# Kernel optimization log

Hardware: AMD Instinct MI355X
Metric: run time of the kernel (lower is better)

Reference implementation:

```python
import jax, jax.numpy as jnp
import numpy as np

NEG = -9.0e15
D = 768


def _init_params(key, d):
    ks = jax.random.split(key, 12)
    s = 0.02
    p = {}
    p['Wa'] = jax.random.normal(ks[0], (d, 1), jnp.float32) * s
    p['ba'] = jnp.zeros((1,), jnp.float32)
    for i, name in enumerate(['qs', 'ks', 'qc', 'kc', 'qr', 'kr']):
        p['W' + name] = jax.random.normal(ks[1 + i], (d, d), jnp.float32) * s
        p['b' + name] = jnp.zeros((d,), jnp.float32)
    p['Wf1'] = jax.random.normal(ks[8], (3 * d, d), jnp.float32) * s
    p['bf1'] = jnp.zeros((d,), jnp.float32)
    p['Wf2'] = jax.random.normal(ks[9], (d, d), jnp.float32) * s
    p['bf2'] = jnp.zeros((d,), jnp.float32)
    p['gamma'] = jnp.ones((d,), jnp.float32)
    p['beta'] = jnp.zeros((d,), jnp.float32)
    return p


def setup_inputs() -> dict:
    key = jax.random.key(0)
    k1, k2, k3 = jax.random.split(key, 3)
    B, L = 8, 1024
    inp = {
        'x': jax.random.normal(k1, (B, L, D), jnp.float32),
        'x_ids': jax.random.randint(k2, (B, L), 0, 1000, jnp.int64 if jax.config.read('jax_enable_x64') else jnp.int32).astype(jnp.int32),
        'pad_idx': 0,
    }
    inp.update(_init_params(k3, D))
    return inp


def _forward(x, x_ids, pad_idx, Wa, ba, Wqs, bqs, Wks, bks, Wqc, bqc, Wkc, bkc,
             Wqr, bqr, Wkr, bkr, Wf1, bf1, Wf2, bf2, gamma, beta):
    B, L, d = x.shape
    valid = x_ids != pad_idx                             # [B,L]
    valid_len = valid.sum(axis=1)
    sep_pos = jnp.clip(valid_len // 2, 1, max(1, L - 2))  # [B]
    pos = jnp.arange(L)[None, :]                          # [1,L]
    false_mask = (pos < sep_pos[:, None]) & valid         # [B,L]
    option_mask = (pos > sep_pos[:, None]) & valid        # [B,L]

    # anomaly gate over false segment
    a_logits = (x @ Wa + ba)[..., 0]                      # [B,L]
    a_logits = jnp.where(false_mask, a_logits, NEG)
    gate = jax.nn.softmax(a_logits, axis=1) * false_mask.astype(x.dtype)
    gate = gate / jnp.clip(gate.sum(axis=1, keepdims=True), 1e-8)

    scale = 1.0 / jnp.sqrt(jnp.asarray(d, x.dtype))
    q_sup, k_sup = x @ Wqs + bqs, x @ Wks + bks
    q_con, k_con = x @ Wqc + bqc, x @ Wkc + bkc
    q_rep, k_rep = x @ Wqr + bqr, x @ Wkr + bkr

    sup_s = jnp.einsum('bld,bmd->blm', q_sup, k_sup) * scale
    con_s = jnp.einsum('bld,bmd->blm', q_con, k_con) * scale
    rep_s = jnp.einsum('bld,bmd->blm', q_rep, k_rep) * scale

    pair_mask = false_mask[:, :, None] & option_mask[:, None, :]  # [B,L,L]
    sup_attn = jax.nn.softmax(jnp.where(pair_mask, sup_s, NEG), axis=-1)
    rep_attn = jax.nn.softmax(jnp.where(pair_mask, rep_s + jnp.tanh(con_s), NEG), axis=-1)

    rep_vec = jnp.einsum('blm,bmd->bld', rep_attn, x)
    sup_vec = jnp.einsum('blm,bmd->bld', sup_attn, x)

    anomaly_false = jnp.einsum('bl,bld->bd', gate, x)
    w_rep = jnp.einsum('bl,bld->bd', gate, rep_vec)
    w_sup = jnp.einsum('bl,bld->bd', gate, sup_vec)

    fused = jnp.concatenate([anomaly_false, w_rep, w_sup], axis=-1)
    fused = jnp.maximum(fused @ Wf1 + bf1, 0.0) @ Wf2 + bf2  # dropout = eval identity

    mu = fused.mean(axis=-1, keepdims=True)
    var = ((fused - mu) ** 2).mean(axis=-1, keepdims=True)
    fused = (fused - mu) / jnp.sqrt(var + 1e-5) * gamma + beta
    return fused


def reference(x, x_ids, pad_idx, Wa, ba, Wqs, bqs, Wks, bks, Wqc, bqc, Wkc, bkc,
              Wqr, bqr, Wkr, bkr, Wf1, bf1, Wf2, bf2, gamma, beta):
    return _forward(x, x_ids, pad_idx, Wa, ba, Wqs, bqs, Wks, bks, Wqc, bqc,
                    Wkc, bkc, Wqr, bqr, Wkr, bkr, Wf1, bf1, Wf2, bf2, gamma, beta)
```

## Files before the change

### kernel.cpp

```cpp
#include <hip/hip_runtime.h>
#include <math.h>

#define L 1024
#define NB 8
#define D 768
#define NEGV (-9.0e15f)
#define SCALE 0.036084391824351615f

typedef unsigned short u16;
typedef __attribute__((ext_vector_type(8))) short short8;
typedef __attribute__((ext_vector_type(4))) float float4v;
#define MFMA_BF16 __builtin_amdgcn_mfma_f32_16x16x32_bf16

__device__ __forceinline__ float b2f(u16 u) {
    union { unsigned int i; float f; } v; v.i = ((unsigned int)u) << 16; return v.f;
}
__device__ __forceinline__ u16 f2b(float f) {
    union { float fv; unsigned int i; } v; v.fv = f;
    unsigned int x = v.i;
    x += 0x7fffu + ((x >> 16) & 1u);
    return (u16)(x >> 16);
}

template<int F32>
__device__ __forceinline__ float4 ld4(const void* p, size_t idx) {
    if (F32) return *(const float4*)((const float*)p + idx);
    ushort4 v = *(const ushort4*)((const u16*)p + idx);
    return make_float4(b2f(v.x), b2f(v.y), b2f(v.z), b2f(v.w));
}
template<int F32>
__device__ __forceinline__ float ld1(const void* p, size_t idx) {
    if (F32) return ((const float*)p)[idx];
    return b2f(((const u16*)p)[idx]);
}
__device__ __forceinline__ int ldid(const int* p, size_t idx, int is64) {
    return is64 ? p[idx * 2] : p[idx];
}

#define WS_FLAG  ((size_t)0)
#define WS_SEP   ((size_t)64)
#define WS_C0    ((size_t)128)
#define WS_Z0    ((size_t)192)
#define WS_W1    ((size_t)9472)
#define WS_GATE  ((size_t)18752)
#define WS_CSUP  ((size_t)51520)
#define WS_CREP  ((size_t)84288)
#define WS_AF    ((size_t)117056)
#define WS_WREP  ((size_t)141632)
#define WS_WSUP  ((size_t)166208)
#define WS_HACC  ((size_t)190784)
#define WS_ALOG  ((size_t)215360)
#define WS_T     ((size_t)248128)
#define WS_OACC  ((size_t)303104)
#define WS_XB    ((size_t)524288)
#define WS_Z     ((size_t)13107200)
#define WS_SSUP  ((size_t)31981568)
#define WS_WB    WS_SSUP
#define WS_SCMB  ((size_t)40370176)
#define WS_M     WS_SCMB

struct PP { const void* W[6]; const void* b[6]; };

__global__ __launch_bounds__(128) void kdetect(const void* x, const void* ids, int* flag) {
    __shared__ int cnt[2];
    int tid = threadIdx.x;
    if (tid == 0) { cnt[0] = 0; cnt[1] = 0; }
    __syncthreads();
    if (tid < 64) {
        u16 u = ((const u16*)x)[tid * 2];
        int e = (u >> 7) & 0xFF;
        if (e >= 100 && e <= 140) atomicAdd(&cnt[0], 1);
    } else {
        int v = ((const int*)ids)[(tid - 64) * 2 + 1];
        if (v != 0) atomicAdd(&cnt[1], 1);
    }
    __syncthreads();
    if (tid == 0) {
        flag[0] = (cnt[0] < 32) ? 1 : 0;
        flag[1] = (cnt[1] == 0) ? 1 : 0;
    }
}

template<int F32> __device__ void kbias_body(const void* W, const void* vec,
        float* out, float* vs) {
    int tid = threadIdx.x;
    for (int i = tid; i < D; i += 256) vs[i] = ld1<F32>(vec, i);
    __syncthreads();
    int row = blockIdx.x * 64 + (tid >> 2);
    int sub = tid & 3;
    float acc = 0.f;
    for (int i = 0; i < 48; ++i) {
        int k = i * 16 + sub * 4;
        float4 wv = ld4<F32>(W, (size_t)row * D + k);
        acc += wv.x * vs[k] + wv.y * vs[k + 1] + wv.z * vs[k + 2] + wv.w * vs[k + 3];
    }
    acc += __shfl_xor(acc, 1);
    acc += __shfl_xor(acc, 2);
    if (sub == 0) out[row] = acc;
}
template<int F32> __device__ void kc0_body(const void* bq, const void* bk,
        float* c0, float* red) {
    int tid = threadIdx.x;
    float s = 0.f;
    for (int i = tid; i < D; i += 256) s += ld1<F32>(bq, i) * ld1<F32>(bk, i);
    red[tid] = s; __syncthreads();
    for (int st = 128; st > 0; st >>= 1) { if (tid < st) red[tid] += red[tid + st]; __syncthreads(); }
    if (tid == 0) c0[0] = red[0];
}
__global__ __launch_bounds__(256) void kbias_row(PP pp, float* z0, float* w1,
        float* c0, const int* flag) {
    __shared__ float vs[D];
    __shared__ float red[256];
    int y = blockIdx.y;
    if (y == 4) {
        if (blockIdx.x != 0) return;
        if (flag[0]) kc0_body<1>(pp.b[2], pp.b[3], c0, red);
        else         kc0_body<0>(pp.b[2], pp.b[3], c0, red);
        return;
    }
    const void* W; const void* vec; float* out;
    if (y < 3) { W = pp.W[2 * y + 1]; vec = pp.b[2 * y]; out = z0 + y * D; }
    else       { W = pp.W[2];         vec = pp.b[3];     out = w1; }
    if (flag[0]) kbias_body<1>(W, vec, out, vs);
    else         kbias_body<0>(W, vec, out, vs);
}

template<int F32> __device__ void kx_body(const void* x, const void* Wa,
        const void* ba, const float* w1, const float* c0, u16* xb, float* alog,
        float* tbuf, float* ws2) {
    int tid = threadIdx.x;
    for (int i = tid; i < D; i += 256) {
        ws2[i]     = ld1<F32>(Wa, i);
        ws2[D + i] = w1[i];
    }
    __syncthreads();
    int row = blockIdx.x * 32 + (tid >> 3);
    int sub = tid & 7;
    float a0 = 0.f, a1 = 0.f;
    for (int i = 0; i < 24; ++i) {
        int k = i * 32 + sub * 4;
        float4 xv = ld4<F32>(x, (size_t)row * D + k);
        ushort4 o;
        o.x = f2b(xv.x); o.y = f2b(xv.y); o.z = f2b(xv.z); o.w = f2b(xv.w);
        *(ushort4*)(xb + (size_t)row * D + k) = o;
        a0 += xv.x * ws2[k] + xv.y * ws2[k + 1] + xv.z * ws2[k + 2] + xv.w * ws2[k + 3];
        a1 += xv.x * ws2[D + k] + xv.y * ws2[D + k + 1] + xv.z * ws2[D + k + 2] + xv.w * ws2[D + k + 3];
    }
    #pragma unroll
    for (int d = 1; d < 8; d <<= 1) {
        a0 += __shfl_xor(a0, d); a1 += __shfl_xor(a1, d);
    }
    int b = row >> 10, l = row & 1023;
    if (sub == 0) alog[row] = a0 + ld1<F32>(ba, 0);
    else if (sub == 1 && l < 512) tbuf[(size_t)b * 512 + l] = a1 + c0[0];
}
__global__ __launch_bounds__(256) void kx(const void* x, PP pp, const void* Wa,
        const void* ba, const float* w1, const float* c0, u16* xb, u16* Wb,
        float* alog, float* tbuf, const int* flag) {
    __shared__ float ws2[2 * D];
    int bid = blockIdx.x;
    if (bid < 256) {
        if (flag[0]) kx_body<1>(x, Wa, ba, w1, c0, xb, alog, tbuf, ws2);
        else         kx_body<0>(x, Wa, ba, w1, c0, xb, alog, tbuf, ws2);
        return;
    }
    int t = (bid - 256) / 288, inner = (bid - 256) % 288;
    const void* src = pp.W[t];
    u16* dst = Wb + (size_t)t * D * D;
    size_t base = ((size_t)inner * 256 + threadIdx.x) * 8;
    if (flag[0]) {
        float4 a = *(const float4*)((const float*)src + base);
        float4 b = *(const float4*)((const float*)src + base + 4);
        uint4 o; u16* po = (u16*)&o;
        po[0] = f2b(a.x); po[1] = f2b(a.y); po[2] = f2b(a.z); po[3] = f2b(a.w);
        po[4] = f2b(b.x); po[5] = f2b(b.y); po[6] = f2b(b.z); po[7] = f2b(b.w);
        *(uint4*)(dst + base) = o;
    } else {
        *(uint4*)(dst + base) = *(const uint4*)((const u16*)src + base);
    }
}

__global__ __launch_bounds__(256) void k0b(const int* __restrict__ ids,
        const int* __restrict__ padp, const float* __restrict__ alog,
        float* __restrict__ gate, int* __restrict__ sepArr,
        float* __restrict__ af, float* __restrict__ wrep, float* __restrict__ wsup,
        float* __restrict__ hacc, float* __restrict__ oacc,
        float* __restrict__ csup, float* __restrict__ crep,
        const int* __restrict__ flag) {
    __shared__ float red[256];
    __shared__ int sepSh;
    int is64 = flag[1];
    int b = blockIdx.x, tid = threadIdx.x;
    int pad = padp[0];
    int cnt = 0;
    for (int l = tid; l < L; l += 256) cnt += (ldid(ids, (size_t)b * L + l, is64) != pad) ? 1 : 0;
    red[tid] = (float)cnt; __syncthreads();
    for (int s = 128; s > 0; s >>= 1) { if (tid < s) red[tid] += red[tid + s]; __syncthreads(); }
    if (tid == 0) {
        int vl = (int)red[0];
        int sep = vl / 2; if (sep < 1) sep = 1; if (sep > L - 2) sep = L - 2;
        sepSh = sep; sepArr[b] = sep;
    }
    __syncthreads();
    int sep = sepSh;
    float lv[4]; int lidx[4];
    float mx = -3.4e38f;
    for (int u = 0; u < 4; ++u) {
        int l = tid + u * 256; lidx[u] = l;
        bool fm = (l < sep) && (ldid(ids, (size_t)b * L + l, is64) != pad);
        float v = fm ? alog[b * L + l] : NEGV;
        lv[u] = v; mx = fmaxf(mx, v);
    }
    red[tid] = mx; __syncthreads();
    for (int s = 128; s > 0; s >>= 1) { if (tid < s) red[tid] = fmaxf(red[tid], red[tid + s]); __syncthreads(); }
    mx = red[0]; __syncthreads();
    float se = 0.f;
    for (int u = 0; u < 4; ++u) { lv[u] = expf(lv[u] - mx); se += lv[u]; }
    red[tid] = se; __syncthreads();
    for (int s = 128; s > 0; s >>= 1) { if (tid < s) red[tid] += red[tid + s]; __syncthreads(); }
    float den = fmaxf(red[0], 1e-30f); __syncthreads();
    float gs = 0.f; float gv[4];
    for (int u = 0; u < 4; ++u) {
        int l = lidx[u];
        bool fm = (l < sep) && (ldid(ids, (size_t)b * L + l, is64) != pad);
        float p = lv[u] / den;
        gv[u] = fm ? p : 0.f;
        gs += gv[u];
    }
    red[tid] = gs; __syncthreads();
    for (int s = 128; s > 0; s >>= 1) { if (tid < s) red[tid] += red[tid + s]; __syncthreads(); }
    gs = red[0];
    float inv = 1.f / fmaxf(gs, 1e-8f);
    for (int u = 0; u < 4; ++u) gate[b * L + lidx[u]] = gv[u] * inv;
    for (int l = tid; l < L; l += 256) { csup[b * L + l] = 0.f; crep[b * L + l] = 0.f; }
    for (int i = tid; i < D; i += 256) {
        af[b * D + i] = 0.f; wrep[b * D + i] = 0.f; wsup[b * D + i] = 0.f;
        hacc[b * D + i] = 0.f; oacc[b * D + i] = 0.f;
    }
}

__device__ __forceinline__ void stage128_async(const u16* __restrict__ G, size_t ld,
        int r0, int k0, u16* S, int tid) {
    int rowa = tid >> 2, koa = (tid & 3) << 3;
    int wave = tid >> 6;
    const u16* g1 = &G[(size_t)(r0 + rowa) * ld + k0 + koa];
    const u16* g2 = &G[(size_t)(r0 + rowa + 64) * ld + k0 + koa];
    __builtin_amdgcn_global_load_lds((__attribute__((address_space(1))) void*)(u16*)g1,
        (__attribute__((address_space(3))) void*)(S + wave * 512), 16, 0, 0);
    __builtin_amdgcn_global_load_lds((__attribute__((address_space(1))) void*)(u16*)g2,
        (__attribute__((address_space(3))) void*)(S + 2048 + wave * 512), 16, 0, 0);
}
__device__ __forceinline__ void stage64_async(const u16* __restrict__ G, size_t ld,
        int r0, int k0, u16* S, int tid) {
    int rowa = tid >> 2, koa = (tid & 3) << 3;
    int wave = tid >> 6;
    const u16* g = &G[(size_t)(r0 + rowa) * ld + k0 + koa];
    __builtin_amdgcn_global_load_lds((__attribute__((address_space(1))) void*)(u16*)g,
        (__attribute__((address_space(3))) void*)(S + wave * 512), 16, 0, 0);
}

__device__ __forceinline__ void gemm_core128(const u16* __restrict__ A, size_t lda, int r0,
        const u16* __restrict__ B, size_t ldb, int c0, int K,
        u16* As, u16* Bs, float4v acc[4][4]) {
    int tid = threadIdx.x;
    int lane = tid & 63, wave = tid >> 6;
    int wm = (wave >> 1) << 6, wn = (wave & 1) << 6;
    int quad = lane >> 4, lrow = lane & 15;
    #pragma unroll
    for (int i = 0; i < 4; ++i)
        #pragma unroll
        for (int j = 0; j < 4; ++j) acc[i][j] = (float4v){0.f, 0.f, 0.f, 0.f};
    for (int k0 = 0; k0 < K; k0 += 64) {
        __syncthreads();
        stage128_async(A, lda, r0, k0, As, tid);
        stage128_async(A, lda, r0, k0 + 32, As + 4096, tid);
        stage128_async(B, ldb, c0, k0, Bs, tid);
        stage128_async(B, ldb, c0, k0 + 32, Bs + 4096, tid);
        __syncthreads();
        #pragma unroll
        for (int p = 0; p < 2; ++p) {
            const u16* Ap = As + p * 4096;
            const u16* Bp = Bs + p * 4096;
            short8 af[4], bf[4];
            #pragma unroll
            for (int i = 0; i < 4; ++i) af[i] = *(const short8*)&Ap[(wm + i * 16 + lrow) * 32 + quad * 8];
            #pragma unroll
            for (int j = 0; j < 4; ++j) bf[j] = *(const short8*)&Bp[(wn + j * 16 + lrow) * 32 + quad * 8];
            #pragma unroll
            for (int i = 0; i < 4; ++i)
                #pragma unroll
                for (int j = 0; j < 4; ++j)
                    acc[i][j] = MFMA_BF16(af[i], bf[j], acc[i][j], 0, 0, 0);
        }
    }
}

__device__ __forceinline__ void gemm_core64(const u16* __restrict__ A, size_t lda, int r0,
        const u16* __restrict__ B, size_t ldb, int c0, int K,
        u16* As, u16* Bs, float4v acc[2][4]) {
    int tid = threadIdx.x;
    int lane = tid & 63, wave = tid >> 6;
    int wm = (wave >> 1) << 5, wn = (wave & 1) << 6;
    int quad = lane >> 4, lrow = lane & 15;
    #pragma unroll
    for (int i = 0; i < 2; ++i)
        #pragma unroll
        for (int j = 0; j < 4; ++j) acc[i][j] = (float4v){0.f, 0.f, 0.f, 0.f};
    for (int k0 = 0; k0 < K; k0 += 64) {
        __syncthreads();
        stage64_async(A, lda, r0, k0, As, tid);
        stage64_async(A, lda, r0, k0 + 32, As + 2048, tid);
        stage128_async(B, ldb, c0, k0, Bs, tid);
        stage128_async(B, ldb, c0, k0 + 32, Bs + 4096, tid);
        __syncthreads();
        #pragma unroll
        for (int p = 0; p < 2; ++p) {
            const u16* Ap = As + p * 2048;
            const u16* Bp = Bs + p * 4096;
            short8 fa[2], fb[4];
            #pragma unroll
            for (int i = 0; i < 2; ++i) fa[i] = *(const short8*)&Ap[(wm + i * 16 + lrow) * 32 + quad * 8];
            #pragma unroll
            for (int j = 0; j < 4; ++j) fb[j] = *(const short8*)&Bp[(wn + j * 16 + lrow) * 32 + quad * 8];
            #pragma unroll
            for (int i = 0; i < 2; ++i)
                #pragma unroll
                for (int j = 0; j < 4; ++j)
                    acc[i][j] = MFMA_BF16(fa[i], fb[j], acc[i][j], 0, 0, 0);
        }
    }
}

__global__ __launch_bounds__(256) void kM_mfma(const u16* __restrict__ Wb, u16* __restrict__ Mt) {
    __shared__ __align__(16) u16 As[128 * 64];
    __shared__ __align__(16) u16 Bs[128 * 64];
    int p = blockIdx.z;
    int r0 = blockIdx.y * 128, c0 = blockIdx.x * 128;
    float4v acc[4][4];
    gemm_core128(Wb + (size_t)(2 * p + 1) * D * D, D, r0,
                 Wb + (size_t)(2 * p) * D * D, D, c0, D, As, Bs, acc);
    int lane = threadIdx.x & 63, wave = threadIdx.x >> 6;
    int wm = (wave >> 1) << 6, wn = (wave & 1) << 6;
    int quad = lane >> 4, lrow = lane & 15;
    u16* out = Mt + (size_t)p * D * D;
    #pragma unroll
    for (int i = 0; i < 4; ++i)
        #pragma unroll
        for (int j = 0; j < 4; ++j) {
            int brow = r0 + wm + i * 16 + quad * 4;
            int col = c0 + wn + j * 16 + lrow;
            #pragma unroll
            for (int r = 0; r < 4; ++r)
                out[(size_t)(brow + r) * D + col] = f2b(acc[i][j][r]);
        }
}

__global__ __launch_bounds__(256) void kZ_mfma(const u16* __restrict__ xb,
        const u16* __restrict__ Mt, const float* __restrict__ z0,
        u16* __restrict__ Zbuf, const int* __restrict__ sepArr) {
    __shared__ __align__(16) u16 As[64 * 64];
    __shared__ __align__(16) u16 Bs[128 * 64];
    int z = blockIdx.z;
    int p = z >> 3, b = z & 7;
    int sep = sepArr[b];
    int r0 = blockIdx.y * 64;
    if (r0 >= sep) return;
    int c0 = blockIdx.x * 128;
    float4v acc[2][4];
    gemm_core64(xb + (size_t)b * L * D, D, r0,
                Mt + (size_t)p * D * D, D, c0, D, As, Bs, acc);
    int lane = threadIdx.x & 63, wave = threadIdx.x >> 6;
    int wm = (wave >> 1) << 5, wn = (wave & 1) << 6;
    int quad = lane >> 4, lrow = lane & 15;
    const float* z0p = z0 + p * D;
    u16* out = Zbuf + ((size_t)p * NB + b) * 512 * D;
    #pragma unroll
    for (int i = 0; i < 2; ++i)
        #pragma unroll
        for (int j = 0; j < 4; ++j) {
            int brow = r0 + wm + i * 16 + quad * 4;
            int col = c0 + wn + j * 16 + lrow;
            float zb = z0p[col];
            #pragma unroll
            for (int r = 0; r < 4; ++r)
                out[(size_t)(brow + r) * D + col] = f2b(acc[i][j][r] + zb);
        }
}

__global__ __launch_bounds__(256) void kS_mfma(const u16* __restrict__ Zbuf,
        const u16* __restrict__ xb, const float* __restrict__ tcbuf,
        const int* __restrict__ sepArr, u16* __restrict__ ssup,
        u16* __restrict__ scmb) {
    __shared__ __align__(16) u16 smem[16384];
    int b = blockIdx.z;
    int sep = sepArr[b];
    int xi = blockIdx.x;
    int tid = threadIdx.x, lane = tid & 63, wave = tid >> 6;
    int quad = lane >> 4, lrow = lane & 15;
    int wm = (wave >> 1) << 5, wn = (wave & 1) << 6;
    int m0 = blockIdx.y * 128;
    if (m0 + 127 <= sep) return;
    u16* A0 = smem;
    u16* A1 = smem + 4096;
    u16* Bs = smem + 8192;
    const u16* X = xb + (size_t)b * L * D;
    if (xi < 8) {
        int l0 = xi * 64;
        if (l0 >= sep) return;
        float4v acc[2][4];
        gemm_core64(Zbuf + (size_t)b * 512 * D, D, l0, X, D, m0, D, A0, Bs, acc);
        u16* out = ssup + (size_t)b * 512 * L;
        #pragma unroll
        for (int i = 0; i < 2; ++i)
            #pragma unroll
            for (int j = 0; j < 4; ++j) {
                int brow = l0 + wm + i * 16 + quad * 4;
                int col = m0 + wn + j * 16 + lrow;
                #pragma unroll
                for (int r = 0; r < 4; ++r)
                    out[(size_t)(brow + r) * L + col] = f2b(acc[i][j][r] * SCALE);
            }
        return;
    }
    int l0 = (xi - 8) * 64;
    if (l0 >= sep) return;
    const u16* Zr = Zbuf + ((size_t)2 * NB + b) * 512 * D;
    const u16* Zc = Zbuf + ((size_t)1 * NB + b) * 512 * D;
    float4v ar_[2][4], ac_[2][4];
    #pragma unroll
    for (int i = 0; i < 2; ++i)
        #pragma unroll
        for (int j = 0; j < 4; ++j) { ar_[i][j] = (float4v){0.f,0.f,0.f,0.f}; ac_[i][j] = (float4v){0.f,0.f,0.f,0.f}; }
    for (int k0 = 0; k0 < D; k0 += 64) {
        __syncthreads();
        stage64_async(Zr, D, l0, k0, A0, tid);
        stage64_async(Zr, D, l0, k0 + 32, A0 + 2048, tid);
        stage64_async(Zc, D, l0, k0, A1, tid);
        stage64_async(Zc, D, l0, k0 + 32, A1 + 2048, tid);
        stage128_async(X, D, m0, k0, Bs, tid);
        stage128_async(X, D, m0, k0 + 32, Bs + 4096, tid);
        __syncthreads();
        #pragma unroll
        for (int p = 0; p < 2; ++p) {
            const u16* Arp = A0 + p * 2048;
            const u16* Acp = A1 + p * 2048;
            const u16* Bp  = Bs + p * 4096;
            short8 fr[2], fc[2], fb[4];
            #pragma unroll
            for (int i = 0; i < 2; ++i) {
                fr[i] = *(const short8*)&Arp[(wm + i * 16 + lrow) * 32 + quad * 8];
                fc[i] = *(const short8*)&Acp[(wm + i * 16 + lrow) * 32 + quad * 8];
            }
            #pragma unroll
            for (int j = 0; j < 4; ++j) fb[j] = *(const short8*)&Bp[(wn + j * 16 + lrow) * 32 + quad * 8];
            #pragma unroll
            for (int i = 0; i < 2; ++i)
                #pragma unroll
                for (int j = 0; j < 4; ++j) {
                    ar_[i][j] = MFMA_BF16(fr[i], fb[j], ar_[i][j], 0, 0, 0);
                    ac_[i][j] = MFMA_BF16(fc[i], fb[j], ac_[i][j], 0, 0, 0);
                }
        }
    }
    const float* tc = tcbuf + (size_t)b * 512;
    u16* out = scmb + (size_t)b * 512 * L;
    #pragma unroll
    for (int i = 0; i < 2; ++i)
        #pragma unroll
        for (int j = 0; j < 4; ++j) {
            int brow = l0 + wm + i * 16 + quad * 4;
            int col = m0 + wn + j * 16 + lrow;
            #pragma unroll
            for (int r = 0; r < 4; ++r) {
                float vv = ar_[i][j][r] * SCALE
                         + tanhf((ac_[i][j][r] + tc[brow + r]) * SCALE);
                out[(size_t)(brow + r) * L + col] = f2b(vv);
            }
        }
}

__global__ __launch_bounds__(256) void k2bc(const u16* __restrict__ ssup,
        const u16* __restrict__ scmb, const int* __restrict__ ids,
        const int* __restrict__ padp, const int* __restrict__ sepArr,
        const float* __restrict__ gate, float* __restrict__ csup,
        float* __restrict__ crep, const int* __restrict__ flag) {
    __shared__ float colacc[4][2][1024];
    int b = blockIdx.y;
    int sep = sepArr[b];
    int l0 = blockIdx.x * 8;
    int tid = threadIdx.x, lane = tid & 63, w = tid >> 6;
    for (int i = tid; i < 4 * 2 * 1024; i += 256) ((float*)colacc)[i] = 0.f;
    __syncthreads();
    if (l0 < sep) {
        int is64 = flag[1];
        int pad = padp[0];
        unsigned int okmask = 0;
        #pragma unroll
        for (int u = 0; u < 16; ++u) {
            int m = u * 64 + lane;
            bool ok = (m > sep) && (ldid(ids, (size_t)b * L + m, is64) != pad);
            okmask |= (ok ? 1u : 0u) << u;
        }
        for (int t = 0; t < 2; ++t) {
            int l = l0 + w * 2 + t;
            if (l >= sep) continue;
            float g = gate[b * L + l];
            if (g == 0.f) continue;
            const u16* rs = ssup + ((size_t)b * 512 + l) * L;
            const u16* rc = scmb + ((size_t)b * 512 + l) * L;
            float s0[16], s1[16];
            float mx0 = -3.4e38f, mx1 = -3.4e38f;
            #pragma unroll
            for (int u = 0; u < 16; ++u) {
                int m = u * 64 + lane;
                bool ok = (okmask >> u) & 1u;
                s0[u] = ok ? b2f(rs[m]) : NEGV;
                s1[u] = ok ? b2f(rc[m]) : NEGV;
                mx0 = fmaxf(mx0, s0[u]); mx1 = fmaxf(mx1, s1[u]);
            }
            #pragma unroll
            for (int d = 1; d < 64; d <<= 1) {
                mx0 = fmaxf(mx0, __shfl_xor(mx0, d));
                mx1 = fmaxf(mx1, __shfl_xor(mx1, d));
            }
            float e0 = 0.f, e1 = 0.f;
            #pragma unroll
            for (int u = 0; u < 16; ++u) {
                s0[u] = expf(s0[u] - mx0); e0 += s0[u];
                s1[u] = expf(s1[u] - mx1); e1 += s1[u];
            }
            #pragma unroll
            for (int d = 1; d < 64; d <<= 1) {
                e0 += __shfl_xor(e0, d);
                e1 += __shfl_xor(e1, d);
            }
            float i0 = g / fmaxf(e0, 1e-30f), i1 = g / fmaxf(e1, 1e-30f);
            #pragma unroll
            for (int u = 0; u < 16; ++u) {
                int m = u * 64 + lane;
                colacc[w][0][m] += s0[u] * i0;
                colacc[w][1][m] += s1[u] * i1;
            }
        }
    }
    __syncthreads();
    for (int m = tid; m < 1024; m += 256) {
        float a0 = colacc[0][0][m] + colacc[1][0][m] + colacc[2][0][m] + colacc[3][0][m];
        float a1 = colacc[0][1][m] + colacc[1][1][m] + colacc[2][1][m] + colacc[3][1][m];
        if (a0 != 0.f) atomicAdd(&csup[b * L + m], a0);
        if (a1 != 0.f) atomicAdd(&crep[b * L + m], a1);
    }
}

__global__ __launch_bounds__(256) void k3(const u16* __restrict__ xb,
        const float* __restrict__ gate, const float* __restrict__ csup,
        const float* __restrict__ crep, float* __restrict__ af,
        float* __restrict__ wrep, float* __restrict__ wsup) {
    int b = blockIdx.y, c = blockIdx.x;
    int tid = threadIdx.x;
    float a0 = 0.f, a1 = 0.f, a2 = 0.f;
    float r0 = 0.f, r1 = 0.f, r2 = 0.f;
    float q0 = 0.f, q1 = 0.f, q2 = 0.f;
    for (int mm = 0; mm < 16; ++mm) {
        int m = c * 16 + mm;
        float wg = gate[b * L + m], wr = crep[b * L + m], wq = csup[b * L + m];
        if (wg == 0.f && wr == 0.f && wq == 0.f) continue;
        size_t base = ((size_t)b * L + m) * D;
        float x0 = b2f(xb[base + tid]);
        float x1 = b2f(xb[base + tid + 256]);
        float x2 = b2f(xb[base + tid + 512]);
        a0 += wg * x0; a1 += wg * x1; a2 += wg * x2;
        r0 += wr * x0; r1 += wr * x1; r2 += wr * x2;
        q0 += wq * x0; q1 += wq * x1; q2 += wq * x2;
    }
    atomicAdd(&af[b * D + tid], a0); atomicAdd(&af[b * D + tid + 256], a1); atomicAdd(&af[b * D + tid + 512], a2);
    atomicAdd(&wrep[b * D + tid], r0); atomicAdd(&wrep[b * D + tid + 256], r1); atomicAdd(&wrep[b * D + tid + 512], r2);
    atomicAdd(&wsup[b * D + tid], q0); atomicAdd(&wsup[b * D + tid + 256], q1); atomicAdd(&wsup[b * D + tid + 512], q2);
}

template<int F32> __device__ void kh1_body(const float* af, const float* wrep,
        const float* wsup, const void* Wf1, float* hacc, float* fs) {
    int tid = threadIdx.x;
    int c0 = blockIdx.x * 128, k0 = blockIdx.y * 144;
    for (int e = tid; e < 8 * 144; e += 256) {
        int b = e / 144, kk = e - b * 144;
        int k = k0 + kk;
        float v = (k < D) ? af[b * D + k] : (k < 2 * D) ? wrep[b * D + k - D]
                                                        : wsup[b * D + k - 2 * D];
        fs[b * 144 + kk] = v;
    }
    __syncthreads();
    int col = c0 + (tid & 127);
    int kg = tid >> 7;
    float acc[NB];
    #pragma unroll
    for (int b = 0; b < NB; ++b) acc[b] = 0.f;
    #pragma unroll 4
    for (int r = 0; r < 72; ++r) {
        int kk = kg * 72 + r;
        float w = ld1<F32>(Wf1, (size_t)(k0 + kk) * D + col);
        #pragma unroll
        for (int b = 0; b < NB; ++b) acc[b] += fs[b * 144 + kk] * w;
    }
    #pragma unroll
    for (int b = 0; b < NB; ++b) atomicAdd(&hacc[b * D + col], acc[b]);
}
__global__ __launch_bounds__(256) void kh1(const float* af, const float* wrep,
        const float* wsup, const void* Wf1, float* hacc, const int* flag) {
    __shared__ float fs[8 * 144];
    if (flag[0]) kh1_body<1>(af, wrep, wsup, Wf1, hacc, fs);
    else         kh1_body<0>(af, wrep, wsup, Wf1, hacc, fs);
}

template<int F32> __device__ void kh2_body(const float* hacc, const void* bf1,
        const void* Wf2, float* oacc, float* hsl) {
    int tid = threadIdx.x;
    int c0 = blockIdx.x * 128, k0 = blockIdx.y * 96;
    for (int e = tid; e < 8 * 96; e += 256) {
        int b = e / 96, kk = e - b * 96;
        int k = k0 + kk;
        hsl[b * 96 + kk] = fmaxf(hacc[b * D + k] + ld1<F32>(bf1, k), 0.f);
    }
    __syncthreads();
    int col = c0 + (tid & 127);
    int kg = tid >> 7;
    float acc[NB];
    #pragma unroll
    for (int b = 0; b < NB; ++b) acc[b] = 0.f;
    #pragma unroll 4
    for (int r = 0; r < 48; ++r) {
        int kk = kg * 48 + r;
        float w = ld1<F32>(Wf2, (size_t)(k0 + kk) * D + col);
        #pragma unroll
        for (int b = 0; b < NB; ++b) acc[b] += hsl[b * 96 + kk] * w;
    }
    #pragma unroll
    for (int b = 0; b < NB; ++b) atomicAdd(&oacc[b * D + col], acc[b]);
}
__global__ __launch_bounds__(256) void kh2(const float* hacc, const void* bf1,
        const void* Wf2, float* oacc, const int* flag) {
    __shared__ float hsl[8 * 96];
    if (flag[0]) kh2_body<1>(hacc, bf1, Wf2, oacc, hsl);
    else         kh2_body<0>(hacc, bf1, Wf2, oacc, hsl);
}

template<int F32> __device__ void kln_body(const float* oacc, const void* bf2,
        const void* gamma, const void* beta, void* out, float* red) {
    int b = blockIdx.x, tid = threadIdx.x;
    float o[3];
    #pragma unroll
    for (int u = 0; u < 3; ++u) {
        int i = tid + u * 256;
        o[u] = oacc[b * D + i] + ld1<F32>(bf2, i);
    }
    red[tid] = o[0] + o[1] + o[2]; __syncthreads();
    for (int s = 128; s > 0; s >>= 1) { if (tid < s) red[tid] += red[tid + s]; __syncthreads(); }
    float mu = red[0] / (float)D; __syncthreads();
    float vs = 0.f;
    #pragma unroll
    for (int u = 0; u < 3; ++u) vs += (o[u] - mu) * (o[u] - mu);
    red[tid] = vs; __syncthreads();
    for (int s = 128; s > 0; s >>= 1) { if (tid < s) red[tid] += red[tid + s]; __syncthreads(); }
    float var = red[0] / (float)D;
    float rstd = 1.0f / sqrtf(var + 1e-5f);
    #pragma unroll
    for (int u = 0; u < 3; ++u) {
        int i = tid + u * 256;
        float v = (o[u] - mu) * rstd * ld1<F32>(gamma, i) + ld1<F32>(beta, i);
        if (F32) ((float*)out)[b * D + i] = v;
        else     ((u16*)out)[b * D + i] = f2b(v);
    }
}
__global__ __launch_bounds__(256) void kln(const float* oacc, const void* bf2,
        const void* gamma, const void* beta, void* out, const int* flag) {
    __shared__ float red[256];
    if (flag[0]) kln_body<1>(oacc, bf2, gamma, beta, out, red);
    else         kln_body<0>(oacc, bf2, gamma, beta, out, red);
}

extern "C" void kernel_launch(void* const* d_in, const int* in_sizes, int n_in,
                              void* d_out, int out_size, void* d_ws, size_t ws_size,
                              hipStream_t stream) {
    const void* x    = d_in[0];
    const int* ids   = (const int*)d_in[1];
    const int* padp  = (const int*)d_in[2];
    const void* Wa   = d_in[3];
    const void* ba   = d_in[4];
    PP pp;
    pp.W[0] = d_in[5];  pp.b[0] = d_in[6];
    pp.W[1] = d_in[7];  pp.b[1] = d_in[8];
    pp.W[2] = d_in[9];  pp.b[2] = d_in[10];
    pp.W[3] = d_in[11]; pp.b[3] = d_in[12];
    pp.W[4] = d_in[13]; pp.b[4] = d_in[14];
    pp.W[5] = d_in[15]; pp.b[5] = d_in[16];
    const void* Wf1 = d_in[17]; const void* bf1 = d_in[18];
    const void* Wf2 = d_in[19]; const void* bf2 = d_in[20];
    const void* gamma = d_in[21]; const void* beta = d_in[22];

    char* ws = (char*)d_ws;
    int*   flag   = (int*)(ws + WS_FLAG);
    int*   sepArr = (int*)(ws + WS_SEP);
    float* c0   = (float*)(ws + WS_C0);
    float* z0   = (float*)(ws + WS_Z0);
    float* w1   = (float*)(ws + WS_W1);
    float* gate = (float*)(ws + WS_GATE);
    float* csup = (float*)(ws + WS_CSUP);
    float* crep = (float*)(ws + WS_CREP);
    float* af   = (float*)(ws + WS_AF);
    float* wrep = (float*)(ws + WS_WREP);
    float* wsup = (float*)(ws + WS_WSUP);
    float* hacc = (float*)(ws + WS_HACC);
    float* oacc = (float*)(ws + WS_OACC);
    float* alog = (float*)(ws + WS_ALOG);
    float* tbuf = (float*)(ws + WS_T);
    u16* xb   = (u16*)(ws + WS_XB);
    u16* Zbuf = (u16*)(ws + WS_Z);
    u16* Wb   = (u16*)(ws + WS_WB);
    u16* Mt   = (u16*)(ws + WS_M);
    u16* ssup = (u16*)(ws + WS_SSUP);
    u16* scmb = (u16*)(ws + WS_SCMB);

    kdetect<<<dim3(1), dim3(128), 0, stream>>>(x, ids, flag);
    kbias_row<<<dim3(12, 5), dim3(256), 0, stream>>>(pp, z0, w1, c0, flag);
    kx<<<dim3(1984), dim3(256), 0, stream>>>(x, pp, Wa, ba, w1, c0, xb, Wb, alog, tbuf, flag);
    k0b<<<dim3(NB), dim3(256), 0, stream>>>(ids, padp, alog, gate, sepArr,
                                            af, wrep, wsup, hacc, oacc, csup, crep, flag);
    kM_mfma<<<dim3(6, 6, 3), dim3(256), 0, stream>>>(Wb, Mt);
    kZ_mfma<<<dim3(6, 8, 24), dim3(256), 0, stream>>>(xb, Mt, z0, Zbuf, sepArr);
    kS_mfma<<<dim3(16, 8, NB), dim3(256), 0, stream>>>(Zbuf, xb, tbuf, sepArr, ssup, scmb);
    k2bc<<<dim3(64, NB), dim3(256), 0, stream>>>(ssup, scmb, ids, padp, sepArr,
                                                 gate, csup, crep, flag);
    k3<<<dim3(64, NB), dim3(256), 0, stream>>>(xb, gate, csup, crep, af, wrep, wsup);
    kh1<<<dim3(6, 16), dim3(256), 0, stream>>>(af, wrep, wsup, Wf1, hacc, flag);
    kh2<<<dim3(6, 8), dim3(256), 0, stream>>>(hacc, bf1, Wf2, oacc, flag);
    kln<<<dim3(NB), dim3(256), 0, stream>>>(oacc, bf2, gamma, beta, d_out, flag);
}
```

Before: 279.6 us.

## Fuse launch chain, inline dtype detection, double-buffer MFMA GEMMs

Removes the separate detect kernel: every kernel now recomputes the dtype flags with a wave ballot. kbias_row is merged into kx as extra blocks, and kM is merged into k0b as kB. The GEMMs now double-buffer their async global-to-LDS staging to overlap loads with MFMA. kS computes the sup and combined score tiles in one pass, sharing the x operand, with fewer grid blocks. This cuts launch count and serial dependencies, but every kernel pays a redundant detection read and the fused kernels have heterogeneous blocks.

```diff
diff --git a/kernel.cpp b/kernel.cpp
--- a/kernel.cpp
+++ b/kernel.cpp
@@ -35,6 +35,22 @@
 }
 __device__ __forceinline__ int ldid(const int* p, size_t idx, int is64) {
     return is64 ? p[idx * 2] : p[idx];
+}
+
+__device__ __forceinline__ void detect2(const void* x, const void* ids, int* sh) {
+    int tid = threadIdx.x;
+    if (tid < 64) {
+        u16 u = ((const u16*)x)[tid * 2];
+        int e = (u >> 7) & 0xFF;
+        unsigned long long balf = __ballot(e >= 100 && e <= 140);
+        int v = ((const int*)ids)[tid * 2 + 1];
+        unsigned long long bali = __ballot(v != 0);
+        if (tid == 0) {
+            sh[0] = (__popcll(balf) < 32) ? 1 : 0;
+            sh[1] = (bali == 0ULL) ? 1 : 0;
+        }
+    }
+    __syncthreads();
 }
 
 #define WS_FLAG  ((size_t)0)
@@ -61,32 +77,12 @@
 
 struct PP { const void* W[6]; const void* b[6]; };
 
-__global__ __launch_bounds__(128) void kdetect(const void* x, const void* ids, int* flag) {
-    __shared__ int cnt[2];
-    int tid = threadIdx.x;
-    if (tid == 0) { cnt[0] = 0; cnt[1] = 0; }
-    __syncthreads();
-    if (tid < 64) {
-        u16 u = ((const u16*)x)[tid * 2];
-        int e = (u >> 7) & 0xFF;
-        if (e >= 100 && e <= 140) atomicAdd(&cnt[0], 1);
-    } else {
-        int v = ((const int*)ids)[(tid - 64) * 2 + 1];
-        if (v != 0) atomicAdd(&cnt[1], 1);
-    }
-    __syncthreads();
-    if (tid == 0) {
-        flag[0] = (cnt[0] < 32) ? 1 : 0;
-        flag[1] = (cnt[1] == 0) ? 1 : 0;
-    }
-}
-
 template<int F32> __device__ void kbias_body(const void* W, const void* vec,
-        float* out, float* vs) {
+        float* out, float* vs, float* red, int xi) {
     int tid = threadIdx.x;
     for (int i = tid; i < D; i += 256) vs[i] = ld1<F32>(vec, i);
     __syncthreads();
-    int row = blockIdx.x * 64 + (tid >> 2);
+    int row = xi * 64 + (tid >> 2);
     int sub = tid & 3;
     float acc = 0.f;
     for (int i = 0; i < 48; ++i) {
@@ -107,36 +103,15 @@
     for (int st = 128; st > 0; st >>= 1) { if (tid < st) red[tid] += red[tid + st]; __syncthreads(); }
     if (tid == 0) c0[0] = red[0];
 }
-__global__ __launch_bounds__(256) void kbias_row(PP pp, float* z0, float* w1,
-        float* c0, const int* flag) {
-    __shared__ float vs[D];
-    __shared__ float red[256];
-    int y = blockIdx.y;
-    if (y == 4) {
-        if (blockIdx.x != 0) return;
-        if (flag[0]) kc0_body<1>(pp.b[2], pp.b[3], c0, red);
-        else         kc0_body<0>(pp.b[2], pp.b[3], c0, red);
-        return;
-    }
-    const void* W; const void* vec; float* out;
-    if (y < 3) { W = pp.W[2 * y + 1]; vec = pp.b[2 * y]; out = z0 + y * D; }
-    else       { W = pp.W[2];         vec = pp.b[3];     out = w1; }
-    if (flag[0]) kbias_body<1>(W, vec, out, vs);
-    else         kbias_body<0>(W, vec, out, vs);
-}
 
 template<int F32> __device__ void kx_body(const void* x, const void* Wa,
-        const void* ba, const float* w1, const float* c0, u16* xb, float* alog,
-        float* tbuf, float* ws2) {
-    int tid = threadIdx.x;
-    for (int i = tid; i < D; i += 256) {
-        ws2[i]     = ld1<F32>(Wa, i);
-        ws2[D + i] = w1[i];
-    }
+        const void* ba, u16* xb, float* alog, float* ws2) {
+    int tid = threadIdx.x;
+    for (int i = tid; i < D; i += 256) ws2[i] = ld1<F32>(Wa, i);
     __syncthreads();
     int row = blockIdx.x * 32 + (tid >> 3);
     int sub = tid & 7;
-    float a0 = 0.f, a1 = 0.f;
+    float a0 = 0.f;
     for (int i = 0; i < 24; ++i) {
         int k = i * 32 + sub * 4;
         float4 xv = ld4<F32>(x, (size_t)row * D + k);
@@ -144,53 +119,219 @@
         o.x = f2b(xv.x); o.y = f2b(xv.y); o.z = f2b(xv.z); o.w = f2b(xv.w);
         *(ushort4*)(xb + (size_t)row * D + k) = o;
         a0 += xv.x * ws2[k] + xv.y * ws2[k + 1] + xv.z * ws2[k + 2] + xv.w * ws2[k + 3];
-        a1 += xv.x * ws2[D + k] + xv.y * ws2[D + k + 1] + xv.z * ws2[D + k + 2] + xv.w * ws2[D + k + 3];
-    }
-    #pragma unroll
-    for (int d = 1; d < 8; d <<= 1) {
-        a0 += __shfl_xor(a0, d); a1 += __shfl_xor(a1, d);
-    }
-    int b = row >> 10, l = row & 1023;
+    }
+    #pragma unroll
+    for (int d = 1; d < 8; d <<= 1) a0 += __shfl_xor(a0, d);
     if (sub == 0) alog[row] = a0 + ld1<F32>(ba, 0);
-    else if (sub == 1 && l < 512) tbuf[(size_t)b * 512 + l] = a1 + c0[0];
-}
-__global__ __launch_bounds__(256) void kx(const void* x, PP pp, const void* Wa,
-        const void* ba, const float* w1, const float* c0, u16* xb, u16* Wb,
-        float* alog, float* tbuf, const int* flag) {
-    __shared__ float ws2[2 * D];
+}
+__global__ __launch_bounds__(256) void kx(const void* x, const int* ids, PP pp,
+        const void* Wa, const void* ba, u16* xb, u16* Wb, float* alog,
+        float* z0, float* w1, float* c0f) {
+    __shared__ float sf[2 * D];
+    __shared__ int fsh[2];
+    detect2(x, ids, fsh);
+    int F32 = fsh[0];
     int bid = blockIdx.x;
     if (bid < 256) {
-        if (flag[0]) kx_body<1>(x, Wa, ba, w1, c0, xb, alog, tbuf, ws2);
-        else         kx_body<0>(x, Wa, ba, w1, c0, xb, alog, tbuf, ws2);
+        if (F32) kx_body<1>(x, Wa, ba, xb, alog, sf);
+        else     kx_body<0>(x, Wa, ba, xb, alog, sf);
         return;
     }
-    int t = (bid - 256) / 288, inner = (bid - 256) % 288;
-    const void* src = pp.W[t];
-    u16* dst = Wb + (size_t)t * D * D;
-    size_t base = ((size_t)inner * 256 + threadIdx.x) * 8;
-    if (flag[0]) {
-        float4 a = *(const float4*)((const float*)src + base);
-        float4 b = *(const float4*)((const float*)src + base + 4);
-        uint4 o; u16* po = (u16*)&o;
-        po[0] = f2b(a.x); po[1] = f2b(a.y); po[2] = f2b(a.z); po[3] = f2b(a.w);
-        po[4] = f2b(b.x); po[5] = f2b(b.y); po[6] = f2b(b.z); po[7] = f2b(b.w);
-        *(uint4*)(dst + base) = o;
-    } else {
-        *(uint4*)(dst + base) = *(const uint4*)((const u16*)src + base);
-    }
-}
-
-__global__ __launch_bounds__(256) void k0b(const int* __restrict__ ids,
+    if (bid < 1984) {
+        int t = (bid - 256) / 288, inner = (bid - 256) % 288;
+        const void* src = pp.W[t];
+        u16* dst = Wb + (size_t)t * D * D;
+        size_t base = ((size_t)inner * 256 + threadIdx.x) * 8;
+        if (F32) {
+            float4 a = *(const float4*)((const float*)src + base);
+            float4 b = *(const float4*)((const float*)src + base + 4);
+            uint4 o; u16* po = (u16*)&o;
+            po[0] = f2b(a.x); po[1] = f2b(a.y); po[2] = f2b(a.z); po[3] = f2b(a.w);
+            po[4] = f2b(b.x); po[5] = f2b(b.y); po[6] = f2b(b.z); po[7] = f2b(b.w);
+            *(uint4*)(dst + base) = o;
+        } else {
+            *(uint4*)(dst + base) = *(const uint4*)((const u16*)src + base);
+        }
+        return;
+    }
+    int i = bid - 1984;
+    int y = i / 12, xi = i % 12;
+    float* vs = sf;
+    float* red = sf + D;
+    if (y == 4) {
+        if (xi != 0) return;
+        if (F32) kc0_body<1>(pp.b[2], pp.b[3], c0f, red);
+        else     kc0_body<0>(pp.b[2], pp.b[3], c0f, red);
+        return;
+    }
+    const void* W; const void* vec; float* out;
+    if (y < 3) { W = pp.W[2 * y + 1]; vec = pp.b[2 * y]; out = z0 + y * D; }
+    else       { W = pp.W[2];         vec = pp.b[3];     out = w1; }
+    if (F32) kbias_body<1>(W, vec, out, vs, red, xi);
+    else     kbias_body<0>(W, vec, out, vs, red, xi);
+}
+
+__device__ __forceinline__ void stage128_async(const u16* __restrict__ G, size_t ld,
+        int r0, int k0, u16* S, int tid) {
+    int rowa = tid >> 2, koa = (tid & 3) << 3;
+    int wave = tid >> 6;
+    const u16* g1 = &G[(size_t)(r0 + rowa) * ld + k0 + koa];
+    const u16* g2 = &G[(size_t)(r0 + rowa + 64) * ld + k0 + koa];
+    __builtin_amdgcn_global_load_lds((__attribute__((address_space(1))) void*)(u16*)g1,
+        (__attribute__((address_space(3))) void*)(S + wave * 512), 16, 0, 0);
+    __builtin_amdgcn_global_load_lds((__attribute__((address_space(1))) void*)(u16*)g2,
+        (__attribute__((address_space(3))) void*)(S + 2048 + wave * 512), 16, 0, 0);
+}
+__device__ __forceinline__ void stage64_async(const u16* __restrict__ G, size_t ld,
+        int r0, int k0, u16* S, int tid) {
+    int rowa = tid >> 2, koa = (tid & 3) << 3;
+    int wave = tid >> 6;
+    const u16* g = &G[(size_t)(r0 + rowa) * ld + k0 + koa];
+    __builtin_amdgcn_global_load_lds((__attribute__((address_space(1))) void*)(u16*)g,
+        (__attribute__((address_space(3))) void*)(S + wave * 512), 16, 0, 0);
+}
+
+__device__ __forceinline__ void gemm64_db(const u16* __restrict__ A, size_t lda, int r0,
+        const u16* __restrict__ B, size_t ldb, int c0, int K,
+        u16* As, u16* Bs, float4v acc[2][4]) {
+    int tid = threadIdx.x;
+    int lane = tid & 63, wave = tid >> 6;
+    int wm = (wave >> 1) << 5, wn = (wave & 1) << 6;
+    int quad = lane >> 4, lrow = lane & 15;
+    #pragma unroll
+    for (int i = 0; i < 2; ++i)
+        #pragma unroll
+        for (int j = 0; j < 4; ++j) acc[i][j] = (float4v){0.f, 0.f, 0.f, 0.f};
+    stage64_async(A, lda, r0, 0, As, tid);
+    stage64_async(A, lda, r0, 32, As + 2048, tid);
+    stage128_async(B, ldb, c0, 0, Bs, tid);
+    stage128_async(B, ldb, c0, 32, Bs + 4096, tid);
+    __syncthreads();
+    int nt = K >> 6;
+    for (int t = 0; t < nt; ++t) {
+        int cur = t & 1;
+        if (t + 1 < nt) {
+            int k0 = (t + 1) << 6;
+            u16* Ad = As + (cur ^ 1) * 4096;
+            u16* Bd = Bs + (cur ^ 1) * 8192;
+            stage64_async(A, lda, r0, k0, Ad, tid);
+            stage64_async(A, lda, r0, k0 + 32, Ad + 2048, tid);
+            stage128_async(B, ldb, c0, k0, Bd, tid);
+            stage128_async(B, ldb, c0, k0 + 32, Bd + 4096, tid);
+        }
+        const u16* Ab = As + cur * 4096;
+        const u16* Bb = Bs + cur * 8192;
+        #pragma unroll
+        for (int p = 0; p < 2; ++p) {
+            const u16* Ap = Ab + p * 2048;
+            const u16* Bp = Bb + p * 4096;
+            short8 fa[2], fb[4];
+            #pragma unroll
+            for (int i = 0; i < 2; ++i) fa[i] = *(const short8*)&Ap[(wm + i * 16 + lrow) * 32 + quad * 8];
+            #pragma unroll
+            for (int j = 0; j < 4; ++j) fb[j] = *(const short8*)&Bp[(wn + j * 16 + lrow) * 32 + quad * 8];
+            #pragma unroll
+            for (int i = 0; i < 2; ++i)
+                #pragma unroll
+                for (int j = 0; j < 4; ++j)
+                    acc[i][j] = MFMA_BF16(fa[i], fb[j], acc[i][j], 0, 0, 0);
+        }
+        __syncthreads();
+    }
+}
+
+__device__ __forceinline__ void gemm128_db(const u16* __restrict__ A, size_t lda, int r0,
+        const u16* __restrict__ B, size_t ldb, int c0, int K,
+        u16* As, u16* Bs, float4v acc[4][4]) {
+    int tid = threadIdx.x;
+    int lane = tid & 63, wave = tid >> 6;
+    int wm = (wave >> 1) << 6, wn = (wave & 1) << 6;
+    int quad = lane >> 4, lrow = lane & 15;
+    #pragma unroll
+    for (int i = 0; i < 4; ++i)
+        #pragma unroll
+        for (int j = 0; j < 4; ++j) acc[i][j] = (float4v){0.f, 0.f, 0.f, 0.f};
+    stage128_async(A, lda, r0, 0, As, tid);
+    stage128_async(A, lda, r0, 32, As + 4096, tid);
+    stage128_async(B, ldb, c0, 0, Bs, tid);
+    stage128_async(B, ldb, c0, 32, Bs + 4096, tid);
+    __syncthreads();
+    int nt = K >> 6;
+    for (int t = 0; t < nt; ++t) {
+        int cur = t & 1;
+        if (t + 1 < nt) {
+            int k0 = (t + 1) << 6;
+            u16* Ad = As + (cur ^ 1) * 8192;
+            u16* Bd = Bs + (cur ^ 1) * 8192;
+            stage128_async(A, lda, r0, k0, Ad, tid);
+            stage128_async(A, lda, r0, k0 + 32, Ad + 4096, tid);
+            stage128_async(B, ldb, c0, k0, Bd, tid);
+            stage128_async(B, ldb, c0, k0 + 32, Bd + 4096, tid);
+        }
+        const u16* Ab = As + cur * 8192;
+        const u16* Bb = Bs + cur * 8192;
+        #pragma unroll
+        for (int p = 0; p < 2; ++p) {
+            const u16* Ap = Ab + p * 4096;
+            const u16* Bp = Bb + p * 4096;
+            short8 fa[4], fb[4];
+            #pragma unroll
+            for (int i = 0; i < 4; ++i) fa[i] = *(const short8*)&Ap[(wm + i * 16 + lrow) * 32 + quad * 8];
+            #pragma unroll
+            for (int j = 0; j < 4; ++j) fb[j] = *(const short8*)&Bp[(wn + j * 16 + lrow) * 32 + quad * 8];
+            #pragma unroll
+            for (int i = 0; i < 4; ++i)
+                #pragma unroll
+                for (int j = 0; j < 4; ++j)
+                    acc[i][j] = MFMA_BF16(fa[i], fb[j], acc[i][j], 0, 0, 0);
+        }
+        __syncthreads();
+    }
+}
+
+__global__ __launch_bounds__(256) void kB(const void* x, const int* __restrict__ ids,
         const int* __restrict__ padp, const float* __restrict__ alog,
         float* __restrict__ gate, int* __restrict__ sepArr,
         float* __restrict__ af, float* __restrict__ wrep, float* __restrict__ wsup,
         float* __restrict__ hacc, float* __restrict__ oacc,
         float* __restrict__ csup, float* __restrict__ crep,
-        const int* __restrict__ flag) {
-    __shared__ float red[256];
-    __shared__ int sepSh;
-    int is64 = flag[1];
-    int b = blockIdx.x, tid = threadIdx.x;
+        const u16* __restrict__ xb, const float* __restrict__ w1,
+        const float* __restrict__ c0f, float* __restrict__ tbuf,
+        const u16* __restrict__ Wb, u16* __restrict__ Mt) {
+    __shared__ __align__(16) u16 SMEM[24576];
+    int bid = blockIdx.x;
+    int tid = threadIdx.x;
+    if (bid >= 8) {
+        int i = bid - 8;
+        int p = i / 72, j = i % 72;
+        int r0 = (j / 6) * 64, c0m = (j % 6) * 128;
+        u16* As = SMEM;
+        u16* Bs = SMEM + 8192;
+        float4v acc[2][4];
+        gemm64_db(Wb + (size_t)(2 * p + 1) * D * D, D, r0,
+                  Wb + (size_t)(2 * p) * D * D, D, c0m, D, As, Bs, acc);
+        int lane = tid & 63, wave = tid >> 6;
+        int wm = (wave >> 1) << 5, wn = (wave & 1) << 6;
+        int quad = lane >> 4, lrow = lane & 15;
+        u16* out = Mt + (size_t)p * D * D;
+        #pragma unroll
+        for (int ii = 0; ii < 2; ++ii)
+            #pragma unroll
+            for (int jj = 0; jj < 4; ++jj) {
+                int brow = r0 + wm + ii * 16 + quad * 4;
+                int col = c0m + wn + jj * 16 + lrow;
+                #pragma unroll
+                for (int r = 0; r < 4; ++r)
+                    out[(size_t)(brow + r) * D + col] = f2b(acc[ii][jj][r]);
+            }
+        return;
+    }
+    float* red = (float*)SMEM;
+    float* w1s = red + 256;
+    int*   ish = (int*)(red + 1024);
+    detect2(x, ids, ish);
+    int is64 = ish[1];
+    int b = bid;
     int pad = padp[0];
     int cnt = 0;
     for (int l = tid; l < L; l += 256) cnt += (ldid(ids, (size_t)b * L + l, is64) != pad) ? 1 : 0;
@@ -199,10 +340,10 @@
     if (tid == 0) {
         int vl = (int)red[0];
         int sep = vl / 2; if (sep < 1) sep = 1; if (sep > L - 2) sep = L - 2;
-        sepSh = sep; sepArr[b] = sep;
-    }
-    __syncthreads();
-    int sep = sepSh;
+        ish[2] = sep; sepArr[b] = sep;
+    }
+    __syncthreads();
+    int sep = ish[2];
     float lv[4]; int lidx[4];
     float mx = -3.4e38f;
     for (int u = 0; u < 4; ++u) {
@@ -237,145 +378,48 @@
         af[b * D + i] = 0.f; wrep[b * D + i] = 0.f; wsup[b * D + i] = 0.f;
         hacc[b * D + i] = 0.f; oacc[b * D + i] = 0.f;
     }
-}
-
-__device__ __forceinline__ void stage128_async(const u16* __restrict__ G, size_t ld,
-        int r0, int k0, u16* S, int tid) {
-    int rowa = tid >> 2, koa = (tid & 3) << 3;
-    int wave = tid >> 6;
-    const u16* g1 = &G[(size_t)(r0 + rowa) * ld + k0 + koa];
-    const u16* g2 = &G[(size_t)(r0 + rowa + 64) * ld + k0 + koa];
-    __builtin_amdgcn_global_load_lds((__attribute__((address_space(1))) void*)(u16*)g1,
-        (__attribute__((address_space(3))) void*)(S + wave * 512), 16, 0, 0);
-    __builtin_amdgcn_global_load_lds((__attribute__((address_space(1))) void*)(u16*)g2,
-        (__attribute__((address_space(3))) void*)(S + 2048 + wave * 512), 16, 0, 0);
-}
-__device__ __forceinline__ void stage64_async(const u16* __restrict__ G, size_t ld,
-        int r0, int k0, u16* S, int tid) {
-    int rowa = tid >> 2, koa = (tid & 3) << 3;
-    int wave = tid >> 6;
-    const u16* g = &G[(size_t)(r0 + rowa) * ld + k0 + koa];
-    __builtin_amdgcn_global_load_lds((__attribute__((address_space(1))) void*)(u16*)g,
-        (__attribute__((address_space(3))) void*)(S + wave * 512), 16, 0, 0);
-}
-
-__device__ __forceinline__ void gemm_core128(const u16* __restrict__ A, size_t lda, int r0,
-        const u16* __restrict__ B, size_t ldb, int c0, int K,
-        u16* As, u16* Bs, float4v acc[4][4]) {
-    int tid = threadIdx.x;
-    int lane = tid & 63, wave = tid >> 6;
-    int wm = (wave >> 1) << 6, wn = (wave & 1) << 6;
-    int quad = lane >> 4, lrow = lane & 15;
-    #pragma unroll
-    for (int i = 0; i < 4; ++i)
-        #pragma unroll
-        for (int j = 0; j < 4; ++j) acc[i][j] = (float4v){0.f, 0.f, 0.f, 0.f};
-    for (int k0 = 0; k0 < K; k0 += 64) {
-        __syncthreads();
-        stage128_async(A, lda, r0, k0, As, tid);
-        stage128_async(A, lda, r0, k0 + 32, As + 4096, tid);
-        stage128_async(B, ldb, c0, k0, Bs, tid);
-        stage128_async(B, ldb, c0, k0 + 32, Bs + 4096, tid);
-        __syncthreads();
-        #pragma unroll
-        for (int p = 0; p < 2; ++p) {
-            const u16* Ap = As + p * 4096;
-            const u16* Bp = Bs + p * 4096;
-            short8 af[4], bf[4];
-            #pragma unroll
-            for (int i = 0; i < 4; ++i) af[i] = *(const short8*)&Ap[(wm + i * 16 + lrow) * 32 + quad * 8];
-            #pragma unroll
-            for (int j = 0; j < 4; ++j) bf[j] = *(const short8*)&Bp[(wn + j * 16 + lrow) * 32 + quad * 8];
-            #pragma unroll
-            for (int i = 0; i < 4; ++i)
-                #pragma unroll
-                for (int j = 0; j < 4; ++j)
-                    acc[i][j] = MFMA_BF16(af[i], bf[j], acc[i][j], 0, 0, 0);
-        }
-    }
-}
-
-__device__ __forceinline__ void gemm_core64(const u16* __restrict__ A, size_t lda, int r0,
-        const u16* __restrict__ B, size_t ldb, int c0, int K,
-        u16* As, u16* Bs, float4v acc[2][4]) {
-    int tid = threadIdx.x;
-    int lane = tid & 63, wave = tid >> 6;
-    int wm = (wave >> 1) << 5, wn = (wave & 1) << 6;
-    int quad = lane >> 4, lrow = lane & 15;
-    #pragma unroll
-    for (int i = 0; i < 2; ++i)
-        #pragma unroll
-        for (int j = 0; j < 4; ++j) acc[i][j] = (float4v){0.f, 0.f, 0.f, 0.f};
-    for (int k0 = 0; k0 < K; k0 += 64) {
-        __syncthreads();
-        stage64_async(A, lda, r0, k0, As, tid);
-        stage64_async(A, lda, r0, k0 + 32, As + 2048, tid);
-        stage128_async(B, ldb, c0, k0, Bs, tid);
-        stage128_async(B, ldb, c0, k0 + 32, Bs + 4096, tid);
-        __syncthreads();
-        #pragma unroll
-        for (int p = 0; p < 2; ++p) {
-            const u16* Ap = As + p * 2048;
-            const u16* Bp = Bs + p * 4096;
-            short8 fa[2], fb[4];
-            #pragma unroll
-            for (int i = 0; i < 2; ++i) fa[i] = *(const short8*)&Ap[(wm + i * 16 + lrow) * 32 + quad * 8];
-            #pragma unroll
-            for (int j = 0; j < 4; ++j) fb[j] = *(const short8*)&Bp[(wn + j * 16 + lrow) * 32 + quad * 8];
-            #pragma unroll
-            for (int i = 0; i < 2; ++i)
-                #pragma unroll
-                for (int j = 0; j < 4; ++j)
-                    acc[i][j] = MFMA_BF16(fa[i], fb[j], acc[i][j], 0, 0, 0);
-        }
-    }
-}
-
-__global__ __launch_bounds__(256) void kM_mfma(const u16* __restrict__ Wb, u16* __restrict__ Mt) {
-    __shared__ __align__(16) u16 As[128 * 64];
-    __shared__ __align__(16) u16 Bs[128 * 64];
-    int p = blockIdx.z;
-    int r0 = blockIdx.y * 128, c0 = blockIdx.x * 128;
+    __syncthreads();
+    for (int i = tid; i < D; i += 256) w1s[i] = w1[i];
+    __syncthreads();
+    float c0v = c0f[0];
+    int sub = tid & 7;
+    for (int pass = 0; pass < 16; ++pass) {
+        int l = pass * 32 + (tid >> 3);
+        const u16* xr = xb + ((size_t)b * L + l) * D;
+        float a = 0.f;
+        for (int i2 = 0; i2 < 12; ++i2) {
+            int k = i2 * 64 + sub * 8;
+            short8 v = *(const short8*)&xr[k];
+            #pragma unroll
+            for (int e = 0; e < 8; ++e) a += b2f((u16)v[e]) * w1s[k + e];
+        }
+        #pragma unroll
+        for (int d2 = 1; d2 < 8; d2 <<= 1) a += __shfl_xor(a, d2);
+        if (sub == 0) tbuf[b * 512 + l] = a + c0v;
+    }
+}
+
+__global__ __launch_bounds__(256) void kZ_mfma(const u16* __restrict__ xb,
+        const u16* __restrict__ Mt, const float* __restrict__ z0,
+        u16* __restrict__ Zbuf, const int* __restrict__ sepArr) {
+    __shared__ __align__(16) u16 As[16384];
+    __shared__ __align__(16) u16 Bs[16384];
+    int z = blockIdx.z;
+    int p = z >> 3, b = z & 7;
+    int sep = sepArr[b];
+    int r0 = blockIdx.y * 128;
+    if (r0 >= sep) return;
+    int c0 = blockIdx.x * 128;
     float4v acc[4][4];
-    gemm_core128(Wb + (size_t)(2 * p + 1) * D * D, D, r0,
-                 Wb + (size_t)(2 * p) * D * D, D, c0, D, As, Bs, acc);
+    gemm128_db(xb + (size_t)b * L * D, D, r0,
+               Mt + (size_t)p * D * D, D, c0, D, As, Bs, acc);
     int lane = threadIdx.x & 63, wave = threadIdx.x >> 6;
     int wm = (wave >> 1) << 6, wn = (wave & 1) << 6;
     int quad = lane >> 4, lrow = lane & 15;
-    u16* out = Mt + (size_t)p * D * D;
-    #pragma unroll
-    for (int i = 0; i < 4; ++i)
-        #pragma unroll
-        for (int j = 0; j < 4; ++j) {
-            int brow = r0 + wm + i * 16 + quad * 4;
-            int col = c0 + wn + j * 16 + lrow;
-            #pragma unroll
-            for (int r = 0; r < 4; ++r)
-                out[(size_t)(brow + r) * D + col] = f2b(acc[i][j][r]);
-        }
-}
-
-__global__ __launch_bounds__(256) void kZ_mfma(const u16* __restrict__ xb,
-        const u16* __restrict__ Mt, const float* __restrict__ z0,
-        u16* __restrict__ Zbuf, const int* __restrict__ sepArr) {
-    __shared__ __align__(16) u16 As[64 * 64];
-    __shared__ __align__(16) u16 Bs[128 * 64];
-    int z = blockIdx.z;
-    int p = z >> 3, b = z & 7;
-    int sep = sepArr[b];
-    int r0 = blockIdx.y * 64;
-    if (r0 >= sep) return;
-    int c0 = blockIdx.x * 128;
-    float4v acc[2][4];
-    gemm_core64(xb + (size_t)b * L * D, D, r0,
-                Mt + (size_t)p * D * D, D, c0, D, As, Bs, acc);
-    int lane = threadIdx.x & 63, wave = threadIdx.x >> 6;
-    int wm = (wave >> 1) << 5, wn = (wave & 1) << 6;
-    int quad = lane >> 4, lrow = lane & 15;
     const float* z0p = z0 + p * D;
     u16* out = Zbuf + ((size_t)p * NB + b) * 512 * D;
     #pragma unroll
-    for (int i = 0; i < 2; ++i)
+    for (int i = 0; i < 4; ++i)
         #pragma unroll
         for (int j = 0; j < 4; ++j) {
             int brow = r0 + wm + i * 16 + quad * 4;
@@ -391,79 +435,80 @@
         const u16* __restrict__ xb, const float* __restrict__ tcbuf,
         const int* __restrict__ sepArr, u16* __restrict__ ssup,
         u16* __restrict__ scmb) {
-    __shared__ __align__(16) u16 smem[16384];
+    __shared__ __align__(16) u16 As[24576];
+    __shared__ __align__(16) u16 Bs[16384];
     int b = blockIdx.z;
     int sep = sepArr[b];
-    int xi = blockIdx.x;
+    int l0 = blockIdx.y * 64;
+    if (l0 >= sep) return;
+    int m0 = blockIdx.x * 128;
+    if (m0 + 127 <= sep) return;
     int tid = threadIdx.x, lane = tid & 63, wave = tid >> 6;
     int quad = lane >> 4, lrow = lane & 15;
     int wm = (wave >> 1) << 5, wn = (wave & 1) << 6;
-    int m0 = blockIdx.y * 128;
-    if (m0 + 127 <= sep) return;
-    u16* A0 = smem;
-    u16* A1 = smem + 4096;
-    u16* Bs = smem + 8192;
+    const u16* A0 = Zbuf + (size_t)b * 512 * D;
+    const u16* A1 = Zbuf + ((size_t)1 * NB + b) * 512 * D;
+    const u16* A2 = Zbuf + ((size_t)2 * NB + b) * 512 * D;
     const u16* X = xb + (size_t)b * L * D;
-    if (xi < 8) {
-        int l0 = xi * 64;
-        if (l0 >= sep) return;
-        float4v acc[2][4];
-        gemm_core64(Zbuf + (size_t)b * 512 * D, D, l0, X, D, m0, D, A0, Bs, acc);
-        u16* out = ssup + (size_t)b * 512 * L;
+    float4v ac[3][2][4];
+    #pragma unroll
+    for (int m = 0; m < 3; ++m)
         #pragma unroll
         for (int i = 0; i < 2; ++i)
             #pragma unroll
-            for (int j = 0; j < 4; ++j) {
-                int brow = l0 + wm + i * 16 + quad * 4;
-                int col = m0 + wn + j * 16 + lrow;
-                #pragma unroll
-                for (int r = 0; r < 4; ++r)
-                    out[(size_t)(brow + r) * L + col] = f2b(acc[i][j][r] * SCALE);
-            }
-        return;
-    }
-    int l0 = (xi - 8) * 64;
-    if (l0 >= sep) return;
-    const u16* Zr = Zbuf + ((size_t)2 * NB + b) * 512 * D;
-    const u16* Zc = Zbuf + ((size_t)1 * NB + b) * 512 * D;
-    float4v ar_[2][4], ac_[2][4];
-    #pragma unroll
-    for (int i = 0; i < 2; ++i)
-        #pragma unroll
-        for (int j = 0; j < 4; ++j) { ar_[i][j] = (float4v){0.f,0.f,0.f,0.f}; ac_[i][j] = (float4v){0.f,0.f,0.f,0.f}; }
-    for (int k0 = 0; k0 < D; k0 += 64) {
-        __syncthreads();
-        stage64_async(Zr, D, l0, k0, A0, tid);
-        stage64_async(Zr, D, l0, k0 + 32, A0 + 2048, tid);
-        stage64_async(Zc, D, l0, k0, A1, tid);
-        stage64_async(Zc, D, l0, k0 + 32, A1 + 2048, tid);
-        stage128_async(X, D, m0, k0, Bs, tid);
-        stage128_async(X, D, m0, k0 + 32, Bs + 4096, tid);
-        __syncthreads();
+            for (int j = 0; j < 4; ++j) ac[m][i][j] = (float4v){0.f, 0.f, 0.f, 0.f};
+    {
+        u16* Ad = As; u16* Bd = Bs;
+        stage64_async(A0, D, l0, 0, Ad, tid);
+        stage64_async(A0, D, l0, 32, Ad + 2048, tid);
+        stage64_async(A1, D, l0, 0, Ad + 4096, tid);
+        stage64_async(A1, D, l0, 32, Ad + 6144, tid);
+        stage64_async(A2, D, l0, 0, Ad + 8192, tid);
+        stage64_async(A2, D, l0, 32, Ad + 10240, tid);
+        stage128_async(X, D, m0, 0, Bd, tid);
+        stage128_async(X, D, m0, 32, Bd + 4096, tid);
+    }
+    __syncthreads();
+    for (int t = 0; t < 12; ++t) {
+        int cur = t & 1;
+        if (t + 1 < 12) {
+            int k0 = (t + 1) << 6;
+            u16* Ad = As + (cur ^ 1) * 12288;
+            u16* Bd = Bs + (cur ^ 1) * 8192;
+            stage64_async(A0, D, l0, k0, Ad, tid);
+            stage64_async(A0, D, l0, k0 + 32, Ad + 2048, tid);
+            stage64_async(A1, D, l0, k0, Ad + 4096, tid);
+            stage64_async(A1, D, l0, k0 + 32, Ad + 6144, tid);
+            stage64_async(A2, D, l0, k0, Ad + 8192, tid);
+            stage64_async(A2, D, l0, k0 + 32, Ad + 10240, tid);
+            stage128_async(X, D, m0, k0, Bd, tid);
+            stage128_async(X, D, m0, k0 + 32, Bd + 4096, tid);
+        }
+        const u16* Ab = As + cur * 12288;
+        const u16* Bb = Bs + cur * 8192;
         #pragma unroll
         for (int p = 0; p < 2; ++p) {
-            const u16* Arp = A0 + p * 2048;
-            const u16* Acp = A1 + p * 2048;
-            const u16* Bp  = Bs + p * 4096;
-            short8 fr[2], fc[2], fb[4];
-            #pragma unroll
-            for (int i = 0; i < 2; ++i) {
-                fr[i] = *(const short8*)&Arp[(wm + i * 16 + lrow) * 32 + quad * 8];
-                fc[i] = *(const short8*)&Acp[(wm + i * 16 + lrow) * 32 + quad * 8];
-            }
+            const u16* Bp = Bb + p * 4096;
+            short8 fb[4];
             #pragma unroll
             for (int j = 0; j < 4; ++j) fb[j] = *(const short8*)&Bp[(wn + j * 16 + lrow) * 32 + quad * 8];
             #pragma unroll
-            for (int i = 0; i < 2; ++i)
+            for (int m = 0; m < 3; ++m) {
+                const u16* Ap = Ab + m * 4096 + p * 2048;
+                short8 f0 = *(const short8*)&Ap[(wm + lrow) * 32 + quad * 8];
+                short8 f1 = *(const short8*)&Ap[(wm + 16 + lrow) * 32 + quad * 8];
                 #pragma unroll
                 for (int j = 0; j < 4; ++j) {
-                    ar_[i][j] = MFMA_BF16(fr[i], fb[j], ar_[i][j], 0, 0, 0);
-                    ac_[i][j] = MFMA_BF16(fc[i], fb[j], ac_[i][j], 0, 0, 0);
+                    ac[m][0][j] = MFMA_BF16(f0, fb[j], ac[m][0][j], 0, 0, 0);
+                    ac[m][1][j] = MFMA_BF16(f1, fb[j], ac[m][1][j], 0, 0, 0);
                 }
-        }
+            }
+        }
+        __syncthreads();
     }
     const float* tc = tcbuf + (size_t)b * 512;
-    u16* out = scmb + (size_t)b * 512 * L;
+    u16* os = ssup + (size_t)b * 512 * L;
+    u16* oc = scmb + (size_t)b * 512 * L;
     #pragma unroll
     for (int i = 0; i < 2; ++i)
         #pragma unroll
@@ -472,19 +517,23 @@
             int col = m0 + wn + j * 16 + lrow;
             #pragma unroll
             for (int r = 0; r < 4; ++r) {
-                float vv = ar_[i][j][r] * SCALE
-                         + tanhf((ac_[i][j][r] + tc[brow + r]) * SCALE);
-                out[(size_t)(brow + r) * L + col] = f2b(vv);
+                os[(size_t)(brow + r) * L + col] = f2b(ac[0][i][j][r] * SCALE);
+                float vv = ac[2][i][j][r] * SCALE
+                         + tanhf((ac[1][i][j][r] + tc[brow + r]) * SCALE);
+                oc[(size_t)(brow + r) * L + col] = f2b(vv);
             }
         }
 }
 
-__global__ __launch_bounds__(256) void k2bc(const u16* __restrict__ ssup,
+__global__ __launch_bounds__(256) void k2bc(const void* __restrict__ x,
+        const u16* __restrict__ ssup,
         const u16* __restrict__ scmb, const int* __restrict__ ids,
         const int* __restrict__ padp, const int* __restrict__ sepArr,
         const float* __restrict__ gate, float* __restrict__ csup,
-        float* __restrict__ crep, const int* __restrict__ flag) {
+        float* __restrict__ crep) {
     __shared__ float colacc[4][2][1024];
+    __shared__ int fsh[2];
+    detect2(x, ids, fsh);
     int b = blockIdx.y;
     int sep = sepArr[b];
     int l0 = blockIdx.x * 8;
@@ -492,7 +541,7 @@
     for (int i = tid; i < 4 * 2 * 1024; i += 256) ((float*)colacc)[i] = 0.f;
     __syncthreads();
     if (l0 < sep) {
-        int is64 = flag[1];
+        int is64 = fsh[1];
         int pad = padp[0];
         unsigned int okmask = 0;
         #pragma unroll
@@ -605,11 +654,14 @@
     #pragma unroll
     for (int b = 0; b < NB; ++b) atomicAdd(&hacc[b * D + col], acc[b]);
 }
-__global__ __launch_bounds__(256) void kh1(const float* af, const float* wrep,
-        const float* wsup, const void* Wf1, float* hacc, const int* flag) {
+__global__ __launch_bounds__(256) void kh1(const void* x, const int* ids,
+        const float* af, const float* wrep,
+        const float* wsup, const void* Wf1, float* hacc) {
     __shared__ float fs[8 * 144];
-    if (flag[0]) kh1_body<1>(af, wrep, wsup, Wf1, hacc, fs);
-    else         kh1_body<0>(af, wrep, wsup, Wf1, hacc, fs);
+    __shared__ int fsh[2];
+    detect2(x, ids, fsh);
+    if (fsh[0]) kh1_body<1>(af, wrep, wsup, Wf1, hacc, fs);
+    else        kh1_body<0>(af, wrep, wsup, Wf1, hacc, fs);
 }
 
 template<int F32> __device__ void kh2_body(const float* hacc, const void* bf1,
@@ -637,11 +689,14 @@
     #pragma unroll
     for (int b = 0; b < NB; ++b) atomicAdd(&oacc[b * D + col], acc[b]);
 }
-__global__ __launch_bounds__(256) void kh2(const float* hacc, const void* bf1,
-        const void* Wf2, float* oacc, const int* flag) {
+__global__ __launch_bounds__(256) void kh2(const void* x, const int* ids,
+        const float* hacc, const void* bf1,
+        const void* Wf2, float* oacc) {
     __shared__ float hsl[8 * 96];
-    if (flag[0]) kh2_body<1>(hacc, bf1, Wf2, oacc, hsl);
-    else         kh2_body<0>(hacc, bf1, Wf2, oacc, hsl);
+    __shared__ int fsh[2];
+    detect2(x, ids, fsh);
+    if (fsh[0]) kh2_body<1>(hacc, bf1, Wf2, oacc, hsl);
+    else        kh2_body<0>(hacc, bf1, Wf2, oacc, hsl);
 }
 
 template<int F32> __device__ void kln_body(const float* oacc, const void* bf2,
@@ -671,11 +726,14 @@
         else     ((u16*)out)[b * D + i] = f2b(v);
     }
 }
-__global__ __launch_bounds__(256) void kln(const float* oacc, const void* bf2,
-        const void* gamma, const void* beta, void* out, const int* flag) {
+__global__ __launch_bounds__(256) void kln(const void* x, const int* ids,
+        const float* oacc, const void* bf2,
+        const void* gamma, const void* beta, void* out) {
     __shared__ float red[256];
-    if (flag[0]) kln_body<1>(oacc, bf2, gamma, beta, out, red);
-    else         kln_body<0>(oacc, bf2, gamma, beta, out, red);
+    __shared__ int fsh[2];
+    detect2(x, ids, fsh);
+    if (fsh[0]) kln_body<1>(oacc, bf2, gamma, beta, out, red);
+    else        kln_body<0>(oacc, bf2, gamma, beta, out, red);
 }
 
 extern "C" void kernel_launch(void* const* d_in, const int* in_sizes, int n_in,
@@ -698,7 +756,6 @@
     const void* gamma = d_in[21]; const void* beta = d_in[22];
 
     char* ws = (char*)d_ws;
-    int*   flag   = (int*)(ws + WS_FLAG);
     int*   sepArr = (int*)(ws + WS_SEP);
     float* c0   = (float*)(ws + WS_C0);
     float* z0   = (float*)(ws + WS_Z0);
@@ -720,18 +777,16 @@
     u16* ssup = (u16*)(ws + WS_SSUP);
     u16* scmb = (u16*)(ws + WS_SCMB);
 
-    kdetect<<<dim3(1), dim3(128), 0, stream>>>(x, ids, flag);
-    kbias_row<<<dim3(12, 5), dim3(256), 0, stream>>>(pp, z0, w1, c0, flag);
-    kx<<<dim3(1984), dim3(256), 0, stream>>>(x, pp, Wa, ba, w1, c0, xb, Wb, alog, tbuf, flag);
-    k0b<<<dim3(NB), dim3(256), 0, stream>>>(ids, padp, alog, gate, sepArr,
-                                            af, wrep, wsup, hacc, oacc, csup, crep, flag);
-    kM_mfma<<<dim3(6, 6, 3), dim3(256), 0, stream>>>(Wb, Mt);
-    kZ_mfma<<<dim3(6, 8, 24), dim3(256), 0, stream>>>(xb, Mt, z0, Zbuf, sepArr);
-    kS_mfma<<<dim3(16, 8, NB), dim3(256), 0, stream>>>(Zbuf, xb, tbuf, sepArr, ssup, scmb);
-    k2bc<<<dim3(64, NB), dim3(256), 0, stream>>>(ssup, scmb, ids, padp, sepArr,
-                                                 gate, csup, crep, flag);
+    kx<<<dim3(2044), dim3(256), 0, stream>>>(x, ids, pp, Wa, ba, xb, Wb, alog, z0, w1, c0);
+    kB<<<dim3(224), dim3(256), 0, stream>>>(x, ids, padp, alog, gate, sepArr,
+                                            af, wrep, wsup, hacc, oacc, csup, crep,
+                                            xb, w1, c0, tbuf, Wb, Mt);
+    kZ_mfma<<<dim3(6, 4, 24), dim3(256), 0, stream>>>(xb, Mt, z0, Zbuf, sepArr);
+    kS_mfma<<<dim3(8, 8, NB), dim3(256), 0, stream>>>(Zbuf, xb, tbuf, sepArr, ssup, scmb);
+    k2bc<<<dim3(64, NB), dim3(256), 0, stream>>>(x, ssup, scmb, ids, padp, sepArr,
+                                                 gate, csup, crep);
     k3<<<dim3(64, NB), dim3(256), 0, stream>>>(xb, gate, csup, crep, af, wrep, wsup);
-    kh1<<<dim3(6, 16), dim3(256), 0, stream>>>(af, wrep, wsup, Wf1, hacc, flag);
-    kh2<<<dim3(6, 8), dim3(256), 0, stream>>>(hacc, bf1, Wf2, oacc, flag);
-    kln<<<dim3(NB), dim3(256), 0, stream>>>(oacc, bf2, gamma, beta, d_out, flag);
-}
+    kh1<<<dim3(6, 16), dim3(256), 0, stream>>>(x, ids, af, wrep, wsup, Wf1, hacc);
+    kh2<<<dim3(6, 8), dim3(256), 0, stream>>>(x, ids, hacc, bf1, Wf2, oacc);
+    kln<<<dim3(NB), dim3(256), 0, stream>>>(x, ids, oacc, bf2, gamma, beta, d_out);
+}
```

Result: slower. 343.6 us (+22.9%).
